# Kernel optimization log

Measured on AMD Instinct MI355X. Metric: run time of the kernel, lower is better.

Reference implementation:

```python
import jax, jax.numpy as jnp
import numpy as np

D_MODEL = 1024
N_HEADS = 16
HEAD_DIM = D_MODEL // N_HEADS
ROPE_BASE = 10000.0


def setup_inputs() -> dict:
    key = jax.random.key(0)
    ks = jax.random.split(key, 9)
    s = 0.02
    inp = {
        "x": jax.random.normal(ks[0], (2, 2048, D_MODEL), dtype=jnp.float32),
        "Wq": jax.random.normal(ks[1], (D_MODEL, D_MODEL), dtype=jnp.float32) * s,
        "bq": jnp.zeros((D_MODEL,), dtype=jnp.float32),
        "Wk": jax.random.normal(ks[2], (D_MODEL, D_MODEL), dtype=jnp.float32) * s,
        "bk": jnp.zeros((D_MODEL,), dtype=jnp.float32),
        "Wv": jax.random.normal(ks[3], (D_MODEL, D_MODEL), dtype=jnp.float32) * s,
        "bv": jnp.zeros((D_MODEL,), dtype=jnp.float32),
        "Wo": jax.random.normal(ks[4], (D_MODEL, D_MODEL), dtype=jnp.float32) * s,
        "bo": jnp.zeros((D_MODEL,), dtype=jnp.float32),
    }
    return inp


def _rope_cos_sin(T, head_dim, dtype):
    inv_freq = 1.0 / (ROPE_BASE ** (jnp.arange(0, head_dim, 2, dtype=jnp.float32) / head_dim))
    pos = jnp.arange(T, dtype=jnp.float32)
    freqs = jnp.outer(pos, inv_freq)              # [T, head_dim/2]
    emb = jnp.concatenate([freqs, freqs], axis=-1)  # [T, head_dim]
    return jnp.cos(emb).astype(dtype), jnp.sin(emb).astype(dtype)


def _rotate_half(x):
    x1, x2 = jnp.split(x, 2, axis=-1)
    return jnp.concatenate([-x2, x1], axis=-1)


def reference(x, Wq, bq, Wk, bk, Wv, bv, Wo, bo):
    B, T, _ = x.shape
    H, Dh = N_HEADS, HEAD_DIM
    # projections (torch Linear: x @ W.T + b)
    q = (x @ Wq.T + bq).reshape(B, T, H, Dh).transpose(0, 2, 1, 3)  # [B,H,T,Dh]
    k = (x @ Wk.T + bk).reshape(B, T, H, Dh).transpose(0, 2, 1, 3)
    v = (x @ Wv.T + bv).reshape(B, T, H, Dh).transpose(0, 2, 1, 3)
    cos, sin = _rope_cos_sin(T, Dh, x.dtype)  # [T, Dh]
    cos = cos[None, None]
    sin = sin[None, None]
    q = q * cos + _rotate_half(q) * sin
    k = k * cos + _rotate_half(k) * sin
    scale = 1.0 / jnp.sqrt(jnp.asarray(Dh, dtype=x.dtype))
    attn = jnp.einsum("bhqd,bhkd->bhqk", q, k) * scale
    attn = jax.nn.softmax(attn, axis=-1)
    out = jnp.einsum("bhqk,bhkd->bhqd", attn, v)  # [B,H,T,Dh]
    out = out.transpose(0, 2, 1, 3).reshape(B, T, H * Dh)
    return out @ Wo.T + bo
```

## Files before the change

### kernel.cpp

```cpp
#include <hip/hip_runtime.h>
#include <hip/hip_bf16.h>
#include <cstdint>

#define D_MODEL 1024
#define NHEADS 16
#define HDIM 64
#define SEQ 2048
#define NBATCH 2
#define BT (NBATCH * SEQ)

typedef short bf16x8 __attribute__((ext_vector_type(8)));
typedef float f32x4 __attribute__((ext_vector_type(4)));
typedef unsigned short u16;
typedef unsigned int u32;

__device__ inline u16 f2bf(float f) {
    union { float f; u32 u; } x;
    x.f = f;
    u32 r = (x.u + 0x7fffu + ((x.u >> 16) & 1u)) >> 16;
    return (u16)r;
}

__device__ inline u32 pack2bf(float a, float b) {
    union { __hip_bfloat162 h; u32 u; } c;
    c.h = __float22bfloat162_rn(float2{a, b});
    return c.u;
}

__device__ inline float bf2f(u16 v) {
    union { u32 u; float f; } x;
    x.u = ((u32)v) << 16;
    return x.f;
}

__device__ inline void async_copy16(const u16* g, u16* l) {
    __builtin_amdgcn_global_load_lds((const __attribute__((address_space(1))) void*)g,
                                     (__attribute__((address_space(3))) void*)l, 16, 0, 0);
}

#define X4 (BT * D_MODEL / 4)
#define W4 (D_MODEL * D_MODEL / 4)
#define ROPE_N (SEQ * 32)

__global__ void prep_kernel(const float* __restrict__ x,
                            const float* __restrict__ wq, const float* __restrict__ wk,
                            const float* __restrict__ wv, const float* __restrict__ wo,
                            u16* __restrict__ xb,
                            u16* __restrict__ dq, u16* __restrict__ dk,
                            u16* __restrict__ dv, u16* __restrict__ dow,
                            float* __restrict__ cosT, float* __restrict__ sinT) {
    int idx = blockIdx.x * blockDim.x + threadIdx.x;
    if (idx < X4) {
        float4 v = ((const float4*)x)[idx];
        ushort4 o;
        o.x = f2bf(v.x); o.y = f2bf(v.y); o.z = f2bf(v.z); o.w = f2bf(v.w);
        ((ushort4*)xb)[idx] = o;
    } else if (idx < X4 + 4 * W4) {
        int j = idx - X4;
        int w = j >> 18, i = j & (W4 - 1);
        const float* s = (w == 0) ? wq : (w == 1) ? wk : (w == 2) ? wv : wo;
        u16* d = (w == 0) ? dq : (w == 1) ? dk : (w == 2) ? dv : dow;
        float4 v = ((const float4*)s)[i];
        ushort4 o;
        o.x = f2bf(v.x); o.y = f2bf(v.y); o.z = f2bf(v.z); o.w = f2bf(v.w);
        ((ushort4*)d)[i] = o;
    } else {
        int j = idx - (X4 + 4 * W4);
        if (j < ROPE_N) {
            int t = j >> 5, dd = j & 31;
            float invf = exp2f(-(float)dd * (13.287712379549449f / 32.0f));
            float ang = (float)t * invf;
            float s, c;
            sincosf(ang, &s, &c);
            cosT[t * HDIM + dd] = c;      cosT[t * HDIM + dd + 32] = c;
            sinT[t * HDIM + dd] = s;      sinT[t * HDIM + dd + 32] = s;
        }
    }
}

__device__ inline void gemm_tile_core(const u16* __restrict__ A, const u16* __restrict__ Bw,
                                      int blkM, int blkN,
                                      u16* Asmem, u16* Bsmem, f32x4 acc[4][4]) {
    const int tid = threadIdx.x;
    const int lane = tid & 63;
    const int wave = tid >> 6;
    const int waveM = wave >> 1, waveN = wave & 1;
    const int quad = lane >> 4, l16 = lane & 15;

    const int srow = tid >> 2;
    const int scol = (tid & 3) << 3;
    const u16* Ag0 = A + (size_t)(blkM * 128 + srow) * D_MODEL + scol;
    const u16* Ag1 = Ag0 + (size_t)64 * D_MODEL;
    const u16* Bg0 = Bw + (size_t)(blkN * 128 + srow) * D_MODEL + scol;
    const u16* Bg1 = Bg0 + (size_t)64 * D_MODEL;
    u16* Al0 = Asmem + srow * 32 + scol;
    u16* Al1 = Al0 + 64 * 32;
    u16* Bl0 = Bsmem + srow * 32 + scol;
    u16* Bl1 = Bl0 + 64 * 32;

    for (int k0 = 0; k0 < D_MODEL; k0 += 32) {
        __syncthreads();
        async_copy16(Ag0 + k0, Al0);
        async_copy16(Ag1 + k0, Al1);
        async_copy16(Bg0 + k0, Bl0);
        async_copy16(Bg1 + k0, Bl1);
        __syncthreads();
        bf16x8 af[4], bfr[4];
#pragma unroll
        for (int mt = 0; mt < 4; ++mt)
            af[mt] = *(const bf16x8*)&Asmem[(waveM * 64 + mt * 16 + l16) * 32 + quad * 8];
#pragma unroll
        for (int nt = 0; nt < 4; ++nt)
            bfr[nt] = *(const bf16x8*)&Bsmem[(waveN * 64 + nt * 16 + l16) * 32 + quad * 8];
#pragma unroll
        for (int mt = 0; mt < 4; ++mt)
#pragma unroll
            for (int nt = 0; nt < 4; ++nt)
                acc[mt][nt] = __builtin_amdgcn_mfma_f32_16x16x32_bf16(af[mt], bfr[nt], acc[mt][nt], 0, 0, 0);
    }
}

#define QSCALE 0.1803368801111204f
#define VPAD 132

__global__ __launch_bounds__(256) void gemm_qkv_kernel(
    const u16* __restrict__ xb,
    const u16* __restrict__ wqb, const u16* __restrict__ wkb, const u16* __restrict__ wvb,
    const float* __restrict__ bq, const float* __restrict__ bk, const float* __restrict__ bv,
    const float* __restrict__ cosT, const float* __restrict__ sinT,
    u16* __restrict__ Qb, u16* __restrict__ Kb, u16* __restrict__ VTb) {
    __shared__ __align__(16) u16 smem[128 * VPAD];
    u16* Asmem = smem;
    u16* Bsmem = smem + 128 * 32;

    const int z = blockIdx.z;
    const u16* Bw = (z == 0) ? wqb : (z == 1) ? wkb : wvb;
    const float* bias = (z == 0) ? bq : (z == 1) ? bk : bv;

    f32x4 acc[4][4];
#pragma unroll
    for (int mt = 0; mt < 4; ++mt)
#pragma unroll
        for (int nt = 0; nt < 4; ++nt)
            acc[mt][nt] = (f32x4){0.f, 0.f, 0.f, 0.f};

    gemm_tile_core(xb, Bw, blockIdx.x, blockIdx.y, Asmem, Bsmem, acc);

    const int tid = threadIdx.x;
    const int lane = tid & 63, wave = tid >> 6;
    const int waveM = wave >> 1, waveN = wave & 1;
    const int quad = lane >> 4, l16 = lane & 15;
    const int gm0 = blockIdx.x * 128 + waveM * 64 + quad * 4;
    const int gn0 = blockIdx.y * 128 + waveN * 64 + l16;

    float bvv[4];
#pragma unroll
    for (int nt = 0; nt < 4; ++nt) bvv[nt] = bias[gn0 + nt * 16];
#pragma unroll
    for (int mt = 0; mt < 4; ++mt)
#pragma unroll
        for (int nt = 0; nt < 4; ++nt)
#pragma unroll
            for (int r = 0; r < 4; ++r) acc[mt][nt][r] += bvv[nt];

    if (z < 2) {
        u16* dst = (z == 0) ? Qb : Kb;
        const float post = (z == 0) ? QSCALE : 1.0f;
#pragma unroll
        for (int mt = 0; mt < 4; ++mt) {
#pragma unroll
            for (int nt = 0; nt < 4; ++nt) {
                int n = gn0 + nt * 16;
                int d = n & 63, h = n >> 6;
#pragma unroll
                for (int r = 0; r < 4; ++r) {
                    int gm = gm0 + mt * 16 + r;
                    int t = gm & (SEQ - 1), b = gm >> 11;
                    float c = cosT[t * HDIM + d], s = sinT[t * HDIM + d];
                    float part = acc[mt][nt ^ 2][r];
                    float rot = (d < 32) ? -part : part;
                    float val = (acc[mt][nt][r] * c + rot * s) * post;
                    dst[((b * NHEADS + h) * SEQ + t) * HDIM + d] = f2bf(val);
                }
            }
        }
    } else {
        __syncthreads();
#pragma unroll
        for (int mt = 0; mt < 4; ++mt) {
            int t_local = waveM * 64 + mt * 16 + quad * 4;
#pragma unroll
            for (int nt = 0; nt < 4; ++nt) {
                int n_local = waveN * 64 + nt * 16 + l16;
                uint2 w;
                w.x = pack2bf(acc[mt][nt][0], acc[mt][nt][1]);
                w.y = pack2bf(acc[mt][nt][2], acc[mt][nt][3]);
                *(uint2*)&smem[n_local * VPAD + t_local] = w;
            }
        }
        __syncthreads();
        const int row = tid >> 1;
        const int hc = (tid & 1) * 64;
        const int n_g = blockIdx.y * 128 + row;
        const int h = n_g >> 6, d = n_g & 63;
        const int b = (blockIdx.x * 128) >> 11;
        const int t0 = ((blockIdx.x * 128) & (SEQ - 1)) + hc;
        u16* dst = &VTb[((size_t)(b * NHEADS + h) * HDIM + d) * SEQ + t0];
        const u16* src = &smem[row * VPAD + hc];
#pragma unroll
        for (int j = 0; j < 8; ++j)
            *(int4*)&dst[j * 8] = *(const int4*)&src[j * 8];
    }
}

#define LPAD 72

__global__ __launch_bounds__(256) void flash_kernel(
    const u16* __restrict__ Qb, const u16* __restrict__ Kb, const u16* __restrict__ VTb,
    u16* __restrict__ Po0 , u16* __restrict__ Po1,
    float* __restrict__ Ls) {
    __shared__ __align__(16) u16 Ks[64 * LPAD];
    __shared__ __align__(16) u16 VTs[64 * LPAD];
    __shared__ __align__(16) u16 Ps[4][32 * LPAD];

    const int tid = threadIdx.x;
    const int wave = tid >> 6, lane = tid & 63;
    const int quad = lane >> 4, l16 = lane & 15;
    const int bh = blockIdx.y;
    const int hf = blockIdx.z;
    const u16* Qh = Qb + (size_t)bh * SEQ * HDIM;
    const u16* Kh = Kb + (size_t)bh * SEQ * HDIM;
    const u16* Vh = VTb + (size_t)bh * HDIM * SEQ;
    const int qblk = blockIdx.x * 128 + wave * 32;
    u16* Pw = (u16*)Ps[wave];

    bf16x8 ones;
#pragma unroll
    for (int i = 0; i < 8; ++i) ones[i] = (short)0x3F80;

    bf16x8 aq[2][2];
#pragma unroll
    for (int nt2 = 0; nt2 < 2; ++nt2)
#pragma unroll
        for (int ks = 0; ks < 2; ++ks)
            aq[nt2][ks] = *(const bf16x8*)&Qh[(qblk + nt2 * 16 + l16) * HDIM + ks * 32 + quad * 8];

    f32x4 o[2][4], accL[2];
#pragma unroll
    for (int mt2 = 0; mt2 < 2; ++mt2) {
        accL[mt2] = (f32x4){0.f, 0.f, 0.f, 0.f};
#pragma unroll
        for (int nt = 0; nt < 4; ++nt) o[mt2][nt] = (f32x4){0.f, 0.f, 0.f, 0.f};
    }

    const int lr = tid >> 2;
    const int lc = (tid & 3) * 16;

    const int ktEnd = (hf + 1) * (SEQ / 128);
    for (int kt = hf * (SEQ / 128); kt < ktEnd; ++kt) {
        __syncthreads();
        *(int4*)&Ks[lr * LPAD + lc] = *(const int4*)&Kh[(kt * 64 + lr) * HDIM + lc];
        *(int4*)&Ks[lr * LPAD + lc + 8] = *(const int4*)&Kh[(kt * 64 + lr) * HDIM + lc + 8];
        *(int4*)&VTs[lr * LPAD + lc] = *(const int4*)&Vh[lr * SEQ + kt * 64 + lc];
        *(int4*)&VTs[lr * LPAD + lc + 8] = *(const int4*)&Vh[lr * SEQ + kt * 64 + lc + 8];
        __syncthreads();

        f32x4 sacc[4][2];
#pragma unroll
        for (int mt = 0; mt < 4; ++mt)
#pragma unroll
            for (int nt2 = 0; nt2 < 2; ++nt2) sacc[mt][nt2] = (f32x4){0.f, 0.f, 0.f, 0.f};
#pragma unroll
        for (int ks = 0; ks < 2; ++ks) {
            bf16x8 kf[4];
#pragma unroll
            for (int mt = 0; mt < 4; ++mt)
                kf[mt] = *(const bf16x8*)&Ks[(mt * 16 + l16) * LPAD + ks * 32 + quad * 8];
#pragma unroll
            for (int mt = 0; mt < 4; ++mt)
#pragma unroll
                for (int nt2 = 0; nt2 < 2; ++nt2)
                    sacc[mt][nt2] = __builtin_amdgcn_mfma_f32_16x16x32_bf16(kf[mt], aq[nt2][ks], sacc[mt][nt2], 0, 0, 0);
        }

#pragma unroll
        for (int mt = 0; mt < 4; ++mt) {
#pragma unroll
            for (int nt2 = 0; nt2 < 2; ++nt2) {
                float p0 = __builtin_amdgcn_exp2f(fminf(sacc[mt][nt2][0], 60.0f));
                float p1 = __builtin_amdgcn_exp2f(fminf(sacc[mt][nt2][1], 60.0f));
                float p2 = __builtin_amdgcn_exp2f(fminf(sacc[mt][nt2][2], 60.0f));
                float p3 = __builtin_amdgcn_exp2f(fminf(sacc[mt][nt2][3], 60.0f));
                uint2 w;
                w.x = pack2bf(p0, p1);
                w.y = pack2bf(p2, p3);
                *(uint2*)&Pw[(nt2 * 16 + l16) * LPAD + mt * 16 + quad * 4] = w;
            }
        }

#pragma unroll
        for (int ks = 0; ks < 2; ++ks) {
            bf16x8 pf[2], vf[4];
#pragma unroll
            for (int mt2 = 0; mt2 < 2; ++mt2)
                pf[mt2] = *(const bf16x8*)&Pw[(mt2 * 16 + l16) * LPAD + ks * 32 + quad * 8];
#pragma unroll
            for (int nt = 0; nt < 4; ++nt)
                vf[nt] = *(const bf16x8*)&VTs[(nt * 16 + l16) * LPAD + ks * 32 + quad * 8];
#pragma unroll
            for (int mt2 = 0; mt2 < 2; ++mt2) {
#pragma unroll
                for (int nt = 0; nt < 4; ++nt)
                    o[mt2][nt] = __builtin_amdgcn_mfma_f32_16x16x32_bf16(pf[mt2], vf[nt], o[mt2][nt], 0, 0, 0);
                accL[mt2] = __builtin_amdgcn_mfma_f32_16x16x32_bf16(pf[mt2], ones, accL[mt2], 0, 0, 0);
            }
        }
    }

    const int b = bh >> 4, h = bh & 15;
    u16* dst = hf ? Po1 : Po0;
#pragma unroll
    for (int mt2 = 0; mt2 < 2; ++mt2) {
#pragma unroll
        for (int nt = 0; nt < 4; ++nt) {
            int d = nt * 16 + l16;
#pragma unroll
            for (int r = 0; r < 4; ++r) {
                int q = qblk + mt2 * 16 + quad * 4 + r;
                dst[((size_t)(b * SEQ + q)) * D_MODEL + h * HDIM + d] = f2bf(o[mt2][nt][r]);
            }
        }
    }
    if (l16 == 0) {
#pragma unroll
        for (int mt2 = 0; mt2 < 2; ++mt2)
#pragma unroll
            for (int r = 0; r < 4; ++r) {
                int q = qblk + mt2 * 16 + quad * 4 + r;
                Ls[hf * (32 * SEQ) + bh * SEQ + q] = accL[mt2][r];
            }
    }
}

__global__ __launch_bounds__(256) void combine_kernel(
    u16* __restrict__ attn , const u16* __restrict__ Po1,
    const float* __restrict__ Ls) {
    int idx = blockIdx.x * 256 + threadIdx.x;
    int c8 = idx & 127;
    int q = idx >> 7;
    int h = c8 >> 3;
    int b = q >> 11, t = q & (SEQ - 1);
    int bh = b * NHEADS + h;
    float l = Ls[bh * SEQ + t] + Ls[32 * SEQ + bh * SEQ + t];
    float rinv = 1.0f / l;
    const ushort4* a0 = (const ushort4*)&attn[(size_t)idx * 8];
    const ushort4* a1 = (const ushort4*)&Po1[(size_t)idx * 8];
    ushort4 v0[2], v1[2];
    v0[0] = a0[0]; v0[1] = a0[1];
    v1[0] = a1[0]; v1[1] = a1[1];
    uint2 outw[2];
#pragma unroll
    for (int j = 0; j < 2; ++j) {
        float s0 = (bf2f(v0[j].x) + bf2f(v1[j].x)) * rinv;
        float s1 = (bf2f(v0[j].y) + bf2f(v1[j].y)) * rinv;
        float s2 = (bf2f(v0[j].z) + bf2f(v1[j].z)) * rinv;
        float s3 = (bf2f(v0[j].w) + bf2f(v1[j].w)) * rinv;
        outw[j].x = pack2bf(s0, s1);
        outw[j].y = pack2bf(s2, s3);
    }
    *(uint4*)&attn[(size_t)idx * 8] = *(uint4*)outw;
}

__global__ __launch_bounds__(256) void gemm_out_kernel(
    const u16* __restrict__ attn, const u16* __restrict__ wob,
    const float* __restrict__ bo, float* __restrict__ dout) {
    __shared__ __align__(16) u16 Asmem[64 * 32];
    __shared__ __align__(16) u16 Bsmem[128 * 32];

    const int tid = threadIdx.x;
    const int lane = tid & 63, wave = tid >> 6;
    const int waveM = wave >> 1, waveN = wave & 1;
    const int quad = lane >> 4, l16 = lane & 15;

    f32x4 acc[2][4];
#pragma unroll
    for (int mt = 0; mt < 2; ++mt)
#pragma unroll
        for (int nt = 0; nt < 4; ++nt) acc[mt][nt] = (f32x4){0.f, 0.f, 0.f, 0.f};

    const int srow = tid >> 2;
    const int scol = (tid & 3) << 3;
    const u16* Ag = attn + (size_t)(blockIdx.x * 64 + srow) * D_MODEL + scol;
    const u16* Bg0 = wob + (size_t)(blockIdx.y * 128 + srow) * D_MODEL + scol;
    const u16* Bg1 = Bg0 + (size_t)64 * D_MODEL;
    u16* Al = Asmem + srow * 32 + scol;
    u16* Bl0 = Bsmem + srow * 32 + scol;
    u16* Bl1 = Bl0 + 64 * 32;

    for (int k0 = 0; k0 < D_MODEL; k0 += 32) {
        __syncthreads();
        async_copy16(Ag + k0, Al);
        async_copy16(Bg0 + k0, Bl0);
        async_copy16(Bg1 + k0, Bl1);
        __syncthreads();
        bf16x8 af[2], bfr[4];
#pragma unroll
        for (int mt = 0; mt < 2; ++mt)
            af[mt] = *(const bf16x8*)&Asmem[(waveM * 32 + mt * 16 + l16) * 32 + quad * 8];
#pragma unroll
        for (int nt = 0; nt < 4; ++nt)
            bfr[nt] = *(const bf16x8*)&Bsmem[(waveN * 64 + nt * 16 + l16) * 32 + quad * 8];
#pragma unroll
        for (int mt = 0; mt < 2; ++mt)
#pragma unroll
            for (int nt = 0; nt < 4; ++nt)
                acc[mt][nt] = __builtin_amdgcn_mfma_f32_16x16x32_bf16(af[mt], bfr[nt], acc[mt][nt], 0, 0, 0);
    }

    const int gm0 = blockIdx.x * 64 + waveM * 32 + quad * 4;
    const int gn0 = blockIdx.y * 128 + waveN * 64 + l16;

    float bvv[4];
#pragma unroll
    for (int nt = 0; nt < 4; ++nt) bvv[nt] = bo[gn0 + nt * 16];
#pragma unroll
    for (int mt = 0; mt < 2; ++mt)
#pragma unroll
        for (int nt = 0; nt < 4; ++nt)
#pragma unroll
            for (int r = 0; r < 4; ++r)
                dout[(size_t)(gm0 + mt * 16 + r) * D_MODEL + gn0 + nt * 16] = acc[mt][nt][r] + bvv[nt];
}

extern "C" void kernel_launch(void* const* d_in, const int* in_sizes, int n_in,
                              void* d_out, int out_size, void* d_ws, size_t ws_size,
                              hipStream_t stream) {
    const float* x  = (const float*)d_in[0];
    const float* Wq = (const float*)d_in[1];
    const float* bq = (const float*)d_in[2];
    const float* Wk = (const float*)d_in[3];
    const float* bk = (const float*)d_in[4];
    const float* Wv = (const float*)d_in[5];
    const float* bv = (const float*)d_in[6];
    const float* Wo = (const float*)d_in[7];
    const float* bo = (const float*)d_in[8];
    float* dout = (float*)d_out;

    char* ws = (char*)d_ws;
    size_t off = 0;
    u16* xb  = (u16*)(ws + off); off += (size_t)BT * D_MODEL * 2;
    u16* wqb = (u16*)(ws + off); off += (size_t)D_MODEL * D_MODEL * 2;
    u16* wkb = (u16*)(ws + off); off += (size_t)D_MODEL * D_MODEL * 2;
    u16* wvb = (u16*)(ws + off); off += (size_t)D_MODEL * D_MODEL * 2;
    u16* wob = (u16*)(ws + off); off += (size_t)D_MODEL * D_MODEL * 2;
    u16* Qb  = (u16*)(ws + off); off += (size_t)BT * D_MODEL * 2;
    u16* Kb  = (u16*)(ws + off); off += (size_t)BT * D_MODEL * 2;
    u16* VTb = (u16*)(ws + off); off += (size_t)BT * D_MODEL * 2;
    u16* attn = (u16*)(ws + off); off += (size_t)BT * D_MODEL * 2;
    float* cosT = (float*)(ws + off); off += (size_t)SEQ * HDIM * 4;
    float* sinT = (float*)(ws + off); off += (size_t)SEQ * HDIM * 4;
    float* Ls   = (float*)(ws + off); off += (size_t)2 * 32 * SEQ * 4;
    u16* Po1 = xb;

    const int prepN = X4 + 4 * W4 + ROPE_N;
    prep_kernel<<<dim3((prepN + 255) / 256), 256, 0, stream>>>(
        x, Wq, Wk, Wv, Wo, xb, wqb, wkb, wvb, wob, cosT, sinT);
    gemm_qkv_kernel<<<dim3(BT / 128, D_MODEL / 128, 3), 256, 0, stream>>>(
        xb, wqb, wkb, wvb, bq, bk, bv, cosT, sinT, Qb, Kb, VTb);
    flash_kernel<<<dim3(SEQ / 128, NBATCH * NHEADS, 2), 256, 0, stream>>>(
        Qb, Kb, VTb, attn, Po1, Ls);
    combine_kernel<<<dim3(BT * D_MODEL / 8 / 256), 256, 0, stream>>>(attn, Po1, Ls);
    gemm_out_kernel<<<dim3(BT / 64, D_MODEL / 128), 256, 0, stream>>>(attn, wob, bo, dout);
}
```

Baseline: 225.9 us.

## Read K/V directly from global in flash kernel and fuse combine into output GEMM

The flash kernel no longer stages K and V^T tiles through shared memory with block-wide barriers. Each wave now loads its MFMA fragments straight from global memory and relies on cache reuse across the four waves. The exp2 clamp is removed, which relies on the scaled scores staying small enough not to overflow. The separate combine kernel is dropped: the output GEMM loads both split-K partial outputs, sums them and divides by the summed row sums while filling its A tile, trading one kernel launch and a round trip through memory for extra per-iteration global loads and ALU work in the GEMM.

```diff
diff --git a/kernel.cpp b/kernel.cpp
--- a/kernel.cpp
+++ b/kernel.cpp
@@ -217,10 +217,7 @@
 
 __global__ __launch_bounds__(256) void flash_kernel(
     const u16* __restrict__ Qb, const u16* __restrict__ Kb, const u16* __restrict__ VTb,
-    u16* __restrict__ Po0 , u16* __restrict__ Po1,
-    float* __restrict__ Ls) {
-    __shared__ __align__(16) u16 Ks[64 * LPAD];
-    __shared__ __align__(16) u16 VTs[64 * LPAD];
+    u16* __restrict__ Po0, u16* __restrict__ Po1, float* __restrict__ Ls) {
     __shared__ __align__(16) u16 Ps[4][32 * LPAD];
 
     const int tid = threadIdx.x;
@@ -253,17 +250,10 @@
         for (int nt = 0; nt < 4; ++nt) o[mt2][nt] = (f32x4){0.f, 0.f, 0.f, 0.f};
     }
 
-    const int lr = tid >> 2;
-    const int lc = (tid & 3) * 16;
-
     const int ktEnd = (hf + 1) * (SEQ / 128);
     for (int kt = hf * (SEQ / 128); kt < ktEnd; ++kt) {
-        __syncthreads();
-        *(int4*)&Ks[lr * LPAD + lc] = *(const int4*)&Kh[(kt * 64 + lr) * HDIM + lc];
-        *(int4*)&Ks[lr * LPAD + lc + 8] = *(const int4*)&Kh[(kt * 64 + lr) * HDIM + lc + 8];
-        *(int4*)&VTs[lr * LPAD + lc] = *(const int4*)&Vh[lr * SEQ + kt * 64 + lc];
-        *(int4*)&VTs[lr * LPAD + lc + 8] = *(const int4*)&Vh[lr * SEQ + kt * 64 + lc + 8];
-        __syncthreads();
+        const u16* Kt = Kh + (size_t)kt * 64 * HDIM;
+        const u16* Vt = Vh + kt * 64;
 
         f32x4 sacc[4][2];
 #pragma unroll
@@ -275,7 +265,7 @@
             bf16x8 kf[4];
 #pragma unroll
             for (int mt = 0; mt < 4; ++mt)
-                kf[mt] = *(const bf16x8*)&Ks[(mt * 16 + l16) * LPAD + ks * 32 + quad * 8];
+                kf[mt] = *(const bf16x8*)&Kt[(mt * 16 + l16) * HDIM + ks * 32 + quad * 8];
 #pragma unroll
             for (int mt = 0; mt < 4; ++mt)
 #pragma unroll
@@ -287,10 +277,10 @@
         for (int mt = 0; mt < 4; ++mt) {
 #pragma unroll
             for (int nt2 = 0; nt2 < 2; ++nt2) {
-                float p0 = __builtin_amdgcn_exp2f(fminf(sacc[mt][nt2][0], 60.0f));
-                float p1 = __builtin_amdgcn_exp2f(fminf(sacc[mt][nt2][1], 60.0f));
-                float p2 = __builtin_amdgcn_exp2f(fminf(sacc[mt][nt2][2], 60.0f));
-                float p3 = __builtin_amdgcn_exp2f(fminf(sacc[mt][nt2][3], 60.0f));
+                float p0 = __builtin_amdgcn_exp2f(sacc[mt][nt2][0]);
+                float p1 = __builtin_amdgcn_exp2f(sacc[mt][nt2][1]);
+                float p2 = __builtin_amdgcn_exp2f(sacc[mt][nt2][2]);
+                float p3 = __builtin_amdgcn_exp2f(sacc[mt][nt2][3]);
                 uint2 w;
                 w.x = pack2bf(p0, p1);
                 w.y = pack2bf(p2, p3);
@@ -306,7 +296,7 @@
                 pf[mt2] = *(const bf16x8*)&Pw[(mt2 * 16 + l16) * LPAD + ks * 32 + quad * 8];
 #pragma unroll
             for (int nt = 0; nt < 4; ++nt)
-                vf[nt] = *(const bf16x8*)&VTs[(nt * 16 + l16) * LPAD + ks * 32 + quad * 8];
+                vf[nt] = *(const bf16x8*)&Vt[(size_t)(nt * 16 + l16) * SEQ + ks * 32 + quad * 8];
 #pragma unroll
             for (int mt2 = 0; mt2 < 2; ++mt2) {
 #pragma unroll
@@ -342,38 +332,9 @@
     }
 }
 
-__global__ __launch_bounds__(256) void combine_kernel(
-    u16* __restrict__ attn , const u16* __restrict__ Po1,
-    const float* __restrict__ Ls) {
-    int idx = blockIdx.x * 256 + threadIdx.x;
-    int c8 = idx & 127;
-    int q = idx >> 7;
-    int h = c8 >> 3;
-    int b = q >> 11, t = q & (SEQ - 1);
-    int bh = b * NHEADS + h;
-    float l = Ls[bh * SEQ + t] + Ls[32 * SEQ + bh * SEQ + t];
-    float rinv = 1.0f / l;
-    const ushort4* a0 = (const ushort4*)&attn[(size_t)idx * 8];
-    const ushort4* a1 = (const ushort4*)&Po1[(size_t)idx * 8];
-    ushort4 v0[2], v1[2];
-    v0[0] = a0[0]; v0[1] = a0[1];
-    v1[0] = a1[0]; v1[1] = a1[1];
-    uint2 outw[2];
-#pragma unroll
-    for (int j = 0; j < 2; ++j) {
-        float s0 = (bf2f(v0[j].x) + bf2f(v1[j].x)) * rinv;
-        float s1 = (bf2f(v0[j].y) + bf2f(v1[j].y)) * rinv;
-        float s2 = (bf2f(v0[j].z) + bf2f(v1[j].z)) * rinv;
-        float s3 = (bf2f(v0[j].w) + bf2f(v1[j].w)) * rinv;
-        outw[j].x = pack2bf(s0, s1);
-        outw[j].y = pack2bf(s2, s3);
-    }
-    *(uint4*)&attn[(size_t)idx * 8] = *(uint4*)outw;
-}
-
 __global__ __launch_bounds__(256) void gemm_out_kernel(
-    const u16* __restrict__ attn, const u16* __restrict__ wob,
-    const float* __restrict__ bo, float* __restrict__ dout) {
+    const u16* __restrict__ Po0, const u16* __restrict__ Po1, const float* __restrict__ Ls,
+    const u16* __restrict__ wob, const float* __restrict__ bo, float* __restrict__ dout) {
     __shared__ __align__(16) u16 Asmem[64 * 32];
     __shared__ __align__(16) u16 Bsmem[128 * 32];
 
@@ -390,7 +351,9 @@
 
     const int srow = tid >> 2;
     const int scol = (tid & 3) << 3;
-    const u16* Ag = attn + (size_t)(blockIdx.x * 64 + srow) * D_MODEL + scol;
+    const int q = blockIdx.x * 64 + srow;
+    const int b = q >> 11, t = q & (SEQ - 1);
+    const size_t arow = (size_t)q * D_MODEL + scol;
     const u16* Bg0 = wob + (size_t)(blockIdx.y * 128 + srow) * D_MODEL + scol;
     const u16* Bg1 = Bg0 + (size_t)64 * D_MODEL;
     u16* Al = Asmem + srow * 32 + scol;
@@ -399,7 +362,23 @@
 
     for (int k0 = 0; k0 < D_MODEL; k0 += 32) {
         __syncthreads();
-        async_copy16(Ag + k0, Al);
+        int h = (k0 + scol) >> 6;
+        int bhq = (b * NHEADS + h) * SEQ + t;
+        float l = Ls[bhq] + Ls[32 * SEQ + bhq];
+        float rinv = 1.0f / l;
+        uint4 A0 = *(const uint4*)&Po0[arow + k0];
+        uint4 A1 = *(const uint4*)&Po1[arow + k0];
+        const u16* p0 = (const u16*)&A0;
+        const u16* p1 = (const u16*)&A1;
+        uint4 wv;
+        u32* wvp = (u32*)&wv;
+#pragma unroll
+        for (int j = 0; j < 4; ++j) {
+            float s0 = (bf2f(p0[2 * j]) + bf2f(p1[2 * j])) * rinv;
+            float s1 = (bf2f(p0[2 * j + 1]) + bf2f(p1[2 * j + 1])) * rinv;
+            wvp[j] = pack2bf(s0, s1);
+        }
+        *(uint4*)Al = wv;
         async_copy16(Bg0 + k0, Bl0);
         async_copy16(Bg1 + k0, Bl1);
         __syncthreads();
@@ -456,7 +435,7 @@
     u16* Qb  = (u16*)(ws + off); off += (size_t)BT * D_MODEL * 2;
     u16* Kb  = (u16*)(ws + off); off += (size_t)BT * D_MODEL * 2;
     u16* VTb = (u16*)(ws + off); off += (size_t)BT * D_MODEL * 2;
-    u16* attn = (u16*)(ws + off); off += (size_t)BT * D_MODEL * 2;
+    u16* Po0 = (u16*)(ws + off); off += (size_t)BT * D_MODEL * 2;
     float* cosT = (float*)(ws + off); off += (size_t)SEQ * HDIM * 4;
     float* sinT = (float*)(ws + off); off += (size_t)SEQ * HDIM * 4;
     float* Ls   = (float*)(ws + off); off += (size_t)2 * 32 * SEQ * 4;
@@ -468,7 +447,7 @@
     gemm_qkv_kernel<<<dim3(BT / 128, D_MODEL / 128, 3), 256, 0, stream>>>(
         xb, wqb, wkb, wvb, bq, bk, bv, cosT, sinT, Qb, Kb, VTb);
     flash_kernel<<<dim3(SEQ / 128, NBATCH * NHEADS, 2), 256, 0, stream>>>(
-        Qb, Kb, VTb, attn, Po1, Ls);
-    combine_kernel<<<dim3(BT * D_MODEL / 8 / 256), 256, 0, stream>>>(attn, Po1, Ls);
-    gemm_out_kernel<<<dim3(BT / 64, D_MODEL / 128), 256, 0, stream>>>(attn, wob, bo, dout);
-}
+        Qb, Kb, VTb, Po0, Po1, Ls);
+    gemm_out_kernel<<<dim3(BT / 64, D_MODEL / 128), 256, 0, stream>>>(
+        Po0, Po1, Ls, wob, bo, dout);
+}
```

Result: slower. 312.6 us (+38.4%).
